# Kernel tuning notes

Hardware: AMD Instinct MI355X
Metric: run time of the kernel (lower is better)

Reference implementation:

```python
import jax, jax.numpy as jnp
import numpy as np

H = 32          # num_attention_heads
ROPE_BASE = 10000.0


def _rotary_freqs_cis(seq_len: int, head_dim: int) -> jnp.ndarray:
    # complex e^{i * pos * theta_j}, shape [seq_len, head_dim//2]
    inv_freq = 1.0 / (ROPE_BASE ** (jnp.arange(0, head_dim, 2, dtype=jnp.float32) / head_dim))
    angles = jnp.arange(seq_len, dtype=jnp.float32)[:, None] * inv_freq[None, :]
    return jax.lax.complex(jnp.cos(angles), jnp.sin(angles))


def _apply_rotary(u: jnp.ndarray, freqs_cis: jnp.ndarray) -> jnp.ndarray:
    # u: [B, S, H, hd]; faithful to apply_rotary_emb (interleaved pairs -> complex mul)
    ur = u.astype(jnp.float32).reshape(*u.shape[:-1], -1, 2)
    uc = jax.lax.complex(ur[..., 0], ur[..., 1])
    # freqs_cis broadcast: [1, S, 1, hd//2]
    uc = uc * freqs_cis[None, :, None, :]
    return jnp.stack((jnp.real(uc), jnp.imag(uc)), axis=-1).reshape(u.shape)


def setup_inputs() -> dict:
    key = jax.random.key(0)
    ks = jax.random.split(key, 5)
    B, S, D = 1, 2048, 4096
    init_std = 0.02
    x = jax.random.normal(ks[0], (B, S, D), dtype=jnp.float32)
    wq = jax.random.normal(ks[1], (D, D), dtype=jnp.float32) * init_std
    wk = jax.random.normal(ks[2], (D, D), dtype=jnp.float32) * init_std
    wv = jax.random.normal(ks[3], (D, D), dtype=jnp.float32) * init_std
    wo = jax.random.normal(ks[4], (D, D), dtype=jnp.float32) * init_std
    return {"x": x, "wq": wq, "wk": wk, "wv": wv, "wo": wo}


def reference(x, wq, wk, wv, wo):
    B, S, D = x.shape
    hd = D // H  # head_dim = 128
    q = (x @ wq).reshape(B, S, H, hd)
    k = (x @ wk).reshape(B, S, H, hd)
    v = (x @ wv).reshape(B, S, H, hd)

    freqs_cis = _rotary_freqs_cis(S, hd)
    q = _apply_rotary(q, freqs_cis)
    k = _apply_rotary(k, freqs_cis)
    # n_rep == 1 (num_key_value_heads == num_attention_heads) -> repeat_kv is identity

    scale = 1.0 / jnp.sqrt(jnp.float32(hd))
    scores = jnp.einsum('bqhd,bkhd->bhqk', q, k) * scale  # [B, H, S, S]
    causal = jnp.tril(jnp.ones((S, S), dtype=bool))
    neg = jnp.finfo(scores.dtype).min
    scores = jnp.where(causal[None, None, :, :], scores, neg)
    probs = jax.nn.softmax(scores, axis=-1)
    attn = jnp.einsum('bhqk,bkhd->bqhd', probs, v).reshape(B, S, D)
    return attn @ wo
```

## Files before the change

kernel.cpp:

```cpp
#include <hip/hip_runtime.h>
#include <stdint.h>

#define S_LEN 2048
#define DMODEL 4096
#define NHEAD 32
#define HDIM 128

typedef __attribute__((ext_vector_type(8))) short bf16x8;
typedef __attribute__((ext_vector_type(4))) float f32x4;

__device__ __forceinline__ unsigned short f2bf(float f) {
    union { float f; unsigned u; } v; v.f = f;
    unsigned u = v.u;
    unsigned r = (u + 0x7FFFu + ((u >> 16) & 1u)) >> 16;
    return (unsigned short)r;
}
__device__ __forceinline__ float bf2f(unsigned short h) {
    union { unsigned u; float f; } v; v.u = ((unsigned)h) << 16;
    return v.f;
}

__global__ void convert_x_kernel(const float* __restrict__ x,
                                 unsigned short* __restrict__ xb, int n4) {
    int t = blockIdx.x * blockDim.x + threadIdx.x;
    if (t >= n4) return;
    float4 v = ((const float4*)x)[t];
    ushort4 o;
    o.x = f2bf(v.x); o.y = f2bf(v.y); o.z = f2bf(v.z); o.w = f2bf(v.w);
    ((ushort4*)xb)[t] = o;
}

__global__ void convert_wt_kernel(const float* __restrict__ w,
                                  unsigned short* __restrict__ wt) {
    __shared__ unsigned short t[64][65];
    int n0 = blockIdx.x * 64, k0 = blockIdx.y * 64;
    for (int i = 0; i < 16; ++i) {
        int o = threadIdx.x + i * 256;
        int r = o >> 6, c = o & 63;
        t[r][c] = f2bf(w[(size_t)(k0 + r) * DMODEL + n0 + c]);
    }
    __syncthreads();
    for (int i = 0; i < 16; ++i) {
        int o = threadIdx.x + i * 256;
        int rr = o >> 6, kk = o & 63;
        wt[(size_t)(n0 + rr) * DMODEL + k0 + kk] = t[kk][rr];
    }
}

template<int STORE_MODE>
__global__ __launch_bounds__(256, 2)
void gemm_bt_kernel(const unsigned short* __restrict__ A,
                    const unsigned short* __restrict__ BT,
                    void* __restrict__ C, int M, int N, int K) {
    __shared__ __align__(16) unsigned short As[128 * 32];
    __shared__ __align__(16) unsigned short Bs[128 * 32];
    const int lane = threadIdx.x & 63;
    const int w = threadIdx.x >> 6;
    const int wm = w & 1, wn = w >> 1;
    const int m0 = blockIdx.y * 128, n0 = blockIdx.x * 128;

    f32x4 zero = {0.f, 0.f, 0.f, 0.f};
    f32x4 acc[4][4];
    for (int i = 0; i < 4; ++i)
        for (int j = 0; j < 4; ++j) acc[i][j] = zero;

    const int lr = lane >> 2;
    const int lc = lane & 3;
    const int q = lane >> 4, lm = lane & 15;

    for (int k0 = 0; k0 < K; k0 += 32) {
        __syncthreads();
        for (int i = 0; i < 2; ++i) {
            int rb = w * 32 + i * 16;
            int r = rb + lr;
            int gc = lc ^ ((r >> 1) & 3);
            const unsigned short* ga = A + (size_t)(m0 + r) * K + k0 + gc * 8;
            __builtin_amdgcn_global_load_lds(
                (__attribute__((address_space(1))) unsigned int*)ga,
                (__attribute__((address_space(3))) unsigned int*)(&As[rb * 32]), 16, 0, 0);
            const unsigned short* gb = BT + (size_t)(n0 + r) * K + k0 + gc * 8;
            __builtin_amdgcn_global_load_lds(
                (__attribute__((address_space(1))) unsigned int*)gb,
                (__attribute__((address_space(3))) unsigned int*)(&Bs[rb * 32]), 16, 0, 0);
        }
        __syncthreads();
        bf16x8 af[4], bf[4];
        for (int t = 0; t < 4; ++t) {
            int ra = wm * 64 + t * 16 + lm;
            af[t] = *(const bf16x8*)&As[ra * 32 + ((q ^ ((ra >> 1) & 3)) * 8)];
            int rb2 = wn * 64 + t * 16 + lm;
            bf[t] = *(const bf16x8*)&Bs[rb2 * 32 + ((q ^ ((rb2 >> 1) & 3)) * 8)];
        }
        for (int mi = 0; mi < 4; ++mi)
            for (int ni = 0; ni < 4; ++ni)
                acc[mi][ni] = __builtin_amdgcn_mfma_f32_16x16x32_bf16(
                    af[mi], bf[ni], acc[mi][ni], 0, 0, 0);
    }

    for (int mi = 0; mi < 4; ++mi) {
        int mbase = m0 + wm * 64 + mi * 16 + q * 4;
        for (int ni = 0; ni < 4; ++ni) {
            int n = n0 + wn * 64 + ni * 16 + lm;
            if (STORE_MODE == 0) {
                unsigned short* Cb = (unsigned short*)C;
                for (int r = 0; r < 4; ++r)
                    Cb[(size_t)(mbase + r) * N + n] = f2bf(acc[mi][ni][r]);
            } else if (STORE_MODE == 1) {
                unsigned short* Cb = (unsigned short*)C;
                ushort4 v;
                v.x = f2bf(acc[mi][ni][0]); v.y = f2bf(acc[mi][ni][1]);
                v.z = f2bf(acc[mi][ni][2]); v.w = f2bf(acc[mi][ni][3]);
                *(ushort4*)&Cb[(size_t)n * M + mbase] = v;
            } else {
                float* Cf = (float*)C;
                for (int r = 0; r < 4; ++r)
                    Cf[(size_t)(mbase + r) * N + n] = acc[mi][ni][r];
            }
        }
    }
}

__global__ void rope_kernel(unsigned short* __restrict__ qb,
                            unsigned short* __restrict__ kb) {
    int t = blockIdx.x * blockDim.x + threadIdx.x;
    if (t >= S_LEN * DMODEL / 2) return;
    int s = t >> 11;
    int p = t & 2047;
    int j = p & 63;
    float ang = (float)s * exp2f((float)j * -0.2076205059304602f);
    float sn, cs;
    sincosf(ang, &sn, &cs);
    size_t idx = (size_t)s * DMODEL + 2 * p;
    const float SC = 0.08838834764831845f;
    float a0 = bf2f(qb[idx]), a1 = bf2f(qb[idx + 1]);
    qb[idx]     = f2bf((a0 * cs - a1 * sn) * SC);
    qb[idx + 1] = f2bf((a0 * sn + a1 * cs) * SC);
    float b0 = bf2f(kb[idx]), b1 = bf2f(kb[idx + 1]);
    kb[idx]     = f2bf(b0 * cs - b1 * sn);
    kb[idx + 1] = f2bf(b0 * sn + b1 * cs);
}

__global__ __launch_bounds__(256, 2)
void attn_kernel(const unsigned short* __restrict__ qb,
                 const unsigned short* __restrict__ kb,
                 const unsigned short* __restrict__ vt,
                 unsigned short* __restrict__ ab) {
    __shared__ __align__(16) unsigned short Ks[64 * 128];
    __shared__ __align__(16) unsigned short VTs[128 * 64];
    __shared__ __align__(16) unsigned short Pb[4][16 * 72];
    const int t = threadIdx.x;
    const int lane = t & 63;
    const int w = t >> 6;
    const int h = blockIdx.y;
    const int q0 = ((int)gridDim.x - 1 - (int)blockIdx.x) * 64;
    const int qw = q0 + w * 16;
    const int q = lane >> 4, lm = lane & 15;

    const int krow = t >> 2;
    const int kcol = t & 3;
    const int vrow = t >> 1;
    const int vcol = t & 1;

    const unsigned short* gK = kb + (size_t)krow * DMODEL + h * HDIM;
    const unsigned short* gV = vt + (size_t)(h * HDIM + vrow) * S_LEN;

    bf16x8 qf[4];
    for (int kc = 0; kc < 4; ++kc)
        qf[kc] = *(const bf16x8*)&qb[(size_t)(qw + lm) * DMODEL + h * HDIM + kc * 32 + q * 8];

    f32x4 zero = {0.f, 0.f, 0.f, 0.f};
    f32x4 o[8];
    for (int i = 0; i < 8; ++i) o[i] = zero;
    float mrow[4] = {-1e30f, -1e30f, -1e30f, -1e30f};
    float lrow[4] = {0.f, 0.f, 0.f, 0.f};

    const int nch = q0 / 64 + 1;

    bf16x8 kreg[4], vreg[4];
    for (int i = 0; i < 4; ++i) {
        kreg[i] = *(const bf16x8*)&gK[(size_t)0 * DMODEL + (kcol + i * 4) * 8];
        vreg[i] = *(const bf16x8*)&gV[0 + (vcol + i * 2) * 8];
    }
    for (int i = 0; i < 4; ++i) {
        *(bf16x8*)&Ks[krow * 128 + (((kcol + i * 4) ^ (krow & 15)) * 8)] = kreg[i];
        *(bf16x8*)&VTs[vrow * 64 + (((vcol + i * 2) ^ (vrow & 7)) * 8)] = vreg[i];
    }
    __syncthreads();

    for (int c = 0; c < nch; ++c) {
        const int j0 = c * 64;
        if (c + 1 < nch) {
            const size_t jn = (size_t)(j0 + 64);
            for (int i = 0; i < 4; ++i) {
                kreg[i] = *(const bf16x8*)&gK[jn * DMODEL + (kcol + i * 4) * 8];
                vreg[i] = *(const bf16x8*)&gV[jn + (vcol + i * 2) * 8];
            }
        }

        f32x4 s[4];
        for (int ks = 0; ks < 4; ++ks) s[ks] = zero;
        for (int kc = 0; kc < 4; ++kc)
            for (int ks = 0; ks < 4; ++ks) {
                bf16x8 kf = *(const bf16x8*)&Ks[(ks * 16 + lm) * 128 + (((kc * 4 + q) ^ lm) * 8)];
                s[ks] = __builtin_amdgcn_mfma_f32_16x16x32_bf16(qf[kc], kf, s[ks], 0, 0, 0);
            }
        if (c == nch - 1) {
            for (int ks = 0; ks < 4; ++ks)
                for (int r = 0; r < 4; ++r)
                    if (j0 + ks * 16 + lm > qw + q * 4 + r) s[ks][r] = -1e30f;
        }
        float al[4];
        for (int r = 0; r < 4; ++r) {
            float mx = fmaxf(fmaxf(s[0][r], s[1][r]), fmaxf(s[2][r], s[3][r]));
            mx = fmaxf(mx, __shfl_xor(mx, 1));
            mx = fmaxf(mx, __shfl_xor(mx, 2));
            mx = fmaxf(mx, __shfl_xor(mx, 4));
            mx = fmaxf(mx, __shfl_xor(mx, 8));
            float mn = fmaxf(mrow[r], mx);
            al[r] = __expf(mrow[r] - mn);
            mrow[r] = mn;
            float rs = 0.f;
            float pv[4];
            for (int ks = 0; ks < 4; ++ks) {
                pv[ks] = __expf(s[ks][r] - mn);
                rs += pv[ks];
            }
            rs += __shfl_xor(rs, 1);
            rs += __shfl_xor(rs, 2);
            rs += __shfl_xor(rs, 4);
            rs += __shfl_xor(rs, 8);
            lrow[r] = lrow[r] * al[r] + rs;
            for (int ks = 0; ks < 4; ++ks)
                Pb[w][(q * 4 + r) * 72 + ks * 16 + lm] = f2bf(pv[ks]);
        }
        bf16x8 pA0 = *(const bf16x8*)&Pb[w][lm * 72 + q * 8];
        bf16x8 pA1 = *(const bf16x8*)&Pb[w][lm * 72 + 32 + q * 8];
        for (int nt = 0; nt < 8; ++nt) {
            int d = nt * 16 + lm;
            bf16x8 vf0 = *(const bf16x8*)&VTs[d * 64 + ((q ^ (d & 7)) * 8)];
            bf16x8 vf1 = *(const bf16x8*)&VTs[d * 64 + (((4 + q) ^ (d & 7)) * 8)];
            f32x4 oo = o[nt];
            for (int r = 0; r < 4; ++r) oo[r] *= al[r];
            oo = __builtin_amdgcn_mfma_f32_16x16x32_bf16(pA0, vf0, oo, 0, 0, 0);
            o[nt] = __builtin_amdgcn_mfma_f32_16x16x32_bf16(pA1, vf1, oo, 0, 0, 0);
        }

        __syncthreads();
        if (c + 1 < nch) {
            for (int i = 0; i < 4; ++i) {
                *(bf16x8*)&Ks[krow * 128 + (((kcol + i * 4) ^ (krow & 15)) * 8)] = kreg[i];
                *(bf16x8*)&VTs[vrow * 64 + (((vcol + i * 2) ^ (vrow & 7)) * 8)] = vreg[i];
            }
        }
        __syncthreads();
    }

    float inv[4];
    for (int r = 0; r < 4; ++r) inv[r] = 1.0f / lrow[r];
    for (int nt = 0; nt < 8; ++nt) {
        int d = h * HDIM + lm + nt * 16;
        for (int r = 0; r < 4; ++r)
            ab[(size_t)(qw + q * 4 + r) * DMODEL + d] = f2bf(o[nt][r] * inv[r]);
    }
}

extern "C" void kernel_launch(void* const* d_in, const int* in_sizes, int n_in,
                              void* d_out, int out_size, void* d_ws, size_t ws_size,
                              hipStream_t stream) {
    const float* x  = (const float*)d_in[0];
    const float* wq = (const float*)d_in[1];
    const float* wk = (const float*)d_in[2];
    const float* wv = (const float*)d_in[3];
    const float* wo = (const float*)d_in[4];
    char* ws = (char*)d_ws;
    const size_t MB = 1024 * 1024;
    unsigned short* xb  = (unsigned short*)(ws + 0 * MB);
    unsigned short* qb  = (unsigned short*)(ws + 16 * MB);
    unsigned short* kb  = (unsigned short*)(ws + 32 * MB);
    unsigned short* vtb = (unsigned short*)(ws + 48 * MB);
    unsigned short* ab  = (unsigned short*)(ws + 64 * MB);
    unsigned short* wtb = (unsigned short*)(ws + 80 * MB);

    dim3 cg(64, 64);
    dim3 gg(32, 16);

    convert_x_kernel<<<(S_LEN * DMODEL / 4) / 256, 256, 0, stream>>>(x, xb, S_LEN * DMODEL / 4);

    convert_wt_kernel<<<cg, 256, 0, stream>>>(wq, wtb);
    gemm_bt_kernel<0><<<gg, 256, 0, stream>>>(xb, wtb, qb, S_LEN, DMODEL, DMODEL);
    convert_wt_kernel<<<cg, 256, 0, stream>>>(wk, wtb);
    gemm_bt_kernel<0><<<gg, 256, 0, stream>>>(xb, wtb, kb, S_LEN, DMODEL, DMODEL);
    convert_wt_kernel<<<cg, 256, 0, stream>>>(wv, wtb);
    gemm_bt_kernel<1><<<gg, 256, 0, stream>>>(xb, wtb, vtb, S_LEN, DMODEL, DMODEL);

    rope_kernel<<<(S_LEN * DMODEL / 2) / 256, 256, 0, stream>>>(qb, kb);

    attn_kernel<<<dim3(S_LEN / 64, NHEAD), 256, 0, stream>>>(qb, kb, vtb, ab);

    convert_wt_kernel<<<cg, 256, 0, stream>>>(wo, wtb);
    gemm_bt_kernel<2><<<gg, 256, 0, stream>>>(ab, wtb, d_out, S_LEN, DMODEL, DMODEL);
}
```

Before: 803.6 us.

## Replace GEMM with 8-wave 256x128 double-buffered ping-pong pipelined kernel

Replaces the simple single-buffered 128x128 bf16 GEMM with a 512-thread kernel that computes 256x128 tiles with K=64 steps. Global-to-LDS loads for the next tiles are issued in stages and overlapped with MFMA phases, using explicit vmcnt waits, barriers, sched_barriers and setprio. Blocks are remapped so that consecutive blocks share B columns. The intent is to hide global load latency and raise MFMA utilisation in all four projection GEMMs. The cost is 96KB of dynamic LDS per block, which limits occupancy, and hand-tuned wait counts that must match the load schedule exactly.

```diff
diff --git a/kernel.cpp b/kernel.cpp
--- a/kernel.cpp
+++ b/kernel.cpp
@@ -47,60 +47,181 @@
     }
 }
 
+
+#define MFMA16(a, b, c) __builtin_amdgcn_mfma_f32_16x16x32_bf16(a, b, c, 0, 0, 0)
+
+#define GLDS(g, l) __builtin_amdgcn_global_load_lds( \
+    (__attribute__((address_space(1))) unsigned int*)(g), \
+    (__attribute__((address_space(3))) unsigned int*)(l), 16, 0, 0)
+
+#define VMCNT_(n) asm volatile("s_waitcnt vmcnt(" #n ")" ::: "memory")
+#define VMCNT(n) VMCNT_(n)
+
+#define PH_SYNC() \
+    __builtin_amdgcn_sched_barrier(0); \
+    __builtin_amdgcn_s_barrier(); \
+    asm volatile("s_waitcnt lgkmcnt(0)" ::: "memory"); \
+    __builtin_amdgcn_sched_barrier(0)
+
+#define PH_END() \
+    __builtin_amdgcn_s_setprio(0); \
+    __builtin_amdgcn_sched_barrier(0); \
+    __builtin_amdgcn_s_barrier(); \
+    __builtin_amdgcn_sched_barrier(0)
+
+#define PH_END_VM(VM) \
+    __builtin_amdgcn_s_setprio(0); \
+    __builtin_amdgcn_sched_barrier(0); \
+    VMCNT(VM); \
+    __builtin_amdgcn_s_barrier(); \
+    __builtin_amdgcn_sched_barrier(0)
+
+#define STAGE_A(T, PAR, J) do { \
+    size_t ko_ = (size_t)(T) * 64 + (J) * 32; \
+    GLDS(gA0 + ko_, As + ((PAR) * 2 + (J)) * 8192 + w * 512); \
+    GLDS(gA1 + ko_, As + ((PAR) * 2 + (J)) * 8192 + 4096 + w * 512); \
+} while (0)
+#define STAGE_B(T, PAR, J) do { \
+    size_t ko_ = (size_t)(T) * 64 + (J) * 32; \
+    GLDS(gB + ko_, Bs + ((PAR) * 2 + (J)) * 4096 + w * 512); \
+} while (0)
+
+#define TILE(T, P, S1, S2, VM2, VM4) do { \
+    const unsigned short* AsT = As + (P) * 16384; \
+    const unsigned short* BsT = Bs + (P) * 8192; \
+    bf16x8 af0, af1, af2, af3, bf0, bf1, bf2, bf3; \
+     \
+    af0 = *(const bf16x8*)&AsT[offA0]; \
+    af1 = *(const bf16x8*)&AsT[offA1]; \
+    af2 = *(const bf16x8*)&AsT[offA2]; \
+    af3 = *(const bf16x8*)&AsT[offA3]; \
+    bf0 = *(const bf16x8*)&BsT[offB0]; \
+    bf1 = *(const bf16x8*)&BsT[offB1]; \
+    if (S1) STAGE_A((T) + 1, (P) ^ 1, 1); \
+    PH_SYNC(); \
+    __builtin_amdgcn_s_setprio(1); \
+    acc[0][0] = MFMA16(af0, bf0, acc[0][0]); \
+    acc[1][0] = MFMA16(af1, bf0, acc[1][0]); \
+    acc[2][0] = MFMA16(af2, bf0, acc[2][0]); \
+    acc[3][0] = MFMA16(af3, bf0, acc[3][0]); \
+    acc[0][1] = MFMA16(af0, bf1, acc[0][1]); \
+    acc[1][1] = MFMA16(af1, bf1, acc[1][1]); \
+    acc[2][1] = MFMA16(af2, bf1, acc[2][1]); \
+    acc[3][1] = MFMA16(af3, bf1, acc[3][1]); \
+    PH_END(); \
+     \
+    bf2 = *(const bf16x8*)&BsT[offB2]; \
+    bf3 = *(const bf16x8*)&BsT[offB3]; \
+    if (S1) STAGE_B((T) + 1, (P) ^ 1, 1); \
+    PH_SYNC(); \
+    __builtin_amdgcn_s_setprio(1); \
+    acc[0][2] = MFMA16(af0, bf2, acc[0][2]); \
+    acc[1][2] = MFMA16(af1, bf2, acc[1][2]); \
+    acc[2][2] = MFMA16(af2, bf2, acc[2][2]); \
+    acc[3][2] = MFMA16(af3, bf2, acc[3][2]); \
+    acc[0][3] = MFMA16(af0, bf3, acc[0][3]); \
+    acc[1][3] = MFMA16(af1, bf3, acc[1][3]); \
+    acc[2][3] = MFMA16(af2, bf3, acc[2][3]); \
+    acc[3][3] = MFMA16(af3, bf3, acc[3][3]); \
+    PH_END_VM(VM2); \
+     \
+    af0 = *(const bf16x8*)&AsT[8192 + offA0]; \
+    af1 = *(const bf16x8*)&AsT[8192 + offA1]; \
+    af2 = *(const bf16x8*)&AsT[8192 + offA2]; \
+    af3 = *(const bf16x8*)&AsT[8192 + offA3]; \
+    bf0 = *(const bf16x8*)&BsT[4096 + offB0]; \
+    bf1 = *(const bf16x8*)&BsT[4096 + offB1]; \
+    if (S2) STAGE_A((T) + 2, (P), 0); \
+    PH_SYNC(); \
+    __builtin_amdgcn_s_setprio(1); \
+    acc[0][0] = MFMA16(af0, bf0, acc[0][0]); \
+    acc[1][0] = MFMA16(af1, bf0, acc[1][0]); \
+    acc[2][0] = MFMA16(af2, bf0, acc[2][0]); \
+    acc[3][0] = MFMA16(af3, bf0, acc[3][0]); \
+    acc[0][1] = MFMA16(af0, bf1, acc[0][1]); \
+    acc[1][1] = MFMA16(af1, bf1, acc[1][1]); \
+    acc[2][1] = MFMA16(af2, bf1, acc[2][1]); \
+    acc[3][1] = MFMA16(af3, bf1, acc[3][1]); \
+    PH_END(); \
+     \
+    bf2 = *(const bf16x8*)&BsT[4096 + offB2]; \
+    bf3 = *(const bf16x8*)&BsT[4096 + offB3]; \
+    if (S2) STAGE_B((T) + 2, (P), 0); \
+    PH_SYNC(); \
+    __builtin_amdgcn_s_setprio(1); \
+    acc[0][2] = MFMA16(af0, bf2, acc[0][2]); \
+    acc[1][2] = MFMA16(af1, bf2, acc[1][2]); \
+    acc[2][2] = MFMA16(af2, bf2, acc[2][2]); \
+    acc[3][2] = MFMA16(af3, bf2, acc[3][2]); \
+    acc[0][3] = MFMA16(af0, bf3, acc[0][3]); \
+    acc[1][3] = MFMA16(af1, bf3, acc[1][3]); \
+    acc[2][3] = MFMA16(af2, bf3, acc[2][3]); \
+    acc[3][3] = MFMA16(af3, bf3, acc[3][3]); \
+    PH_END_VM(VM4); \
+} while (0)
+
 template<int STORE_MODE>
-__global__ __launch_bounds__(256, 2)
-void gemm_bt_kernel(const unsigned short* __restrict__ A,
-                    const unsigned short* __restrict__ BT,
-                    void* __restrict__ C, int M, int N, int K) {
-    __shared__ __align__(16) unsigned short As[128 * 32];
-    __shared__ __align__(16) unsigned short Bs[128 * 32];
-    const int lane = threadIdx.x & 63;
-    const int w = threadIdx.x >> 6;
-    const int wm = w & 1, wn = w >> 1;
-    const int m0 = blockIdx.y * 128, n0 = blockIdx.x * 128;
+__global__ __launch_bounds__(512, 2)
+void gemm8p_kernel(const unsigned short* __restrict__ A,
+                   const unsigned short* __restrict__ BT,
+                   void* __restrict__ C) {
+    constexpr int M = S_LEN, N = DMODEL, K = DMODEL;
+    constexpr int NT = K / 64;
+    extern __shared__ __align__(16) unsigned short sm[];
+    unsigned short* As = sm;
+    unsigned short* Bs = sm + 32768;
+
+    const int tid = threadIdx.x;
+    const int lane = tid & 63;
+    const int w = tid >> 6;
+    const int wr = w >> 1, wc = w & 1;
+    const int q = lane >> 4, lm = lane & 15;
+
+    int orig = blockIdx.y * gridDim.x + blockIdx.x;
+    const int by = orig & 7;
+    const int bx = orig >> 3;
+    const int m0 = by * 256, n0 = bx * 128;
+
+    const int c4 = tid & 3, r4 = tid >> 2, s4 = (tid >> 3) & 3;
+    const unsigned short* gA0 = A + (size_t)(m0 + r4) * K + ((c4 ^ s4) * 8);
+    const unsigned short* gA1 = gA0 + (size_t)128 * K;
+    const unsigned short* gB  = BT + (size_t)(n0 + r4) * K + ((c4 ^ s4) * 8);
+
+#define FRAGOFF(r_) ((r_) * 32 + ((q ^ (((r_) >> 1) & 3)) * 8))
+    const int rA = wr * 64 + lm, rB = wc * 64 + lm;
+    const int offA0 = FRAGOFF(rA);
+    const int offA1 = FRAGOFF(rA + 16);
+    const int offA2 = FRAGOFF(rA + 32);
+    const int offA3 = FRAGOFF(rA + 48);
+    const int offB0 = FRAGOFF(rB);
+    const int offB1 = FRAGOFF(rB + 16);
+    const int offB2 = FRAGOFF(rB + 32);
+    const int offB3 = FRAGOFF(rB + 48);
+#undef FRAGOFF
 
     f32x4 zero = {0.f, 0.f, 0.f, 0.f};
     f32x4 acc[4][4];
     for (int i = 0; i < 4; ++i)
         for (int j = 0; j < 4; ++j) acc[i][j] = zero;
 
-    const int lr = lane >> 2;
-    const int lc = lane & 3;
-    const int q = lane >> 4, lm = lane & 15;
-
-    for (int k0 = 0; k0 < K; k0 += 32) {
-        __syncthreads();
-        for (int i = 0; i < 2; ++i) {
-            int rb = w * 32 + i * 16;
-            int r = rb + lr;
-            int gc = lc ^ ((r >> 1) & 3);
-            const unsigned short* ga = A + (size_t)(m0 + r) * K + k0 + gc * 8;
-            __builtin_amdgcn_global_load_lds(
-                (__attribute__((address_space(1))) unsigned int*)ga,
-                (__attribute__((address_space(3))) unsigned int*)(&As[rb * 32]), 16, 0, 0);
-            const unsigned short* gb = BT + (size_t)(n0 + r) * K + k0 + gc * 8;
-            __builtin_amdgcn_global_load_lds(
-                (__attribute__((address_space(1))) unsigned int*)gb,
-                (__attribute__((address_space(3))) unsigned int*)(&Bs[rb * 32]), 16, 0, 0);
-        }
-        __syncthreads();
-        bf16x8 af[4], bf[4];
-        for (int t = 0; t < 4; ++t) {
-            int ra = wm * 64 + t * 16 + lm;
-            af[t] = *(const bf16x8*)&As[ra * 32 + ((q ^ ((ra >> 1) & 3)) * 8)];
-            int rb2 = wn * 64 + t * 16 + lm;
-            bf[t] = *(const bf16x8*)&Bs[rb2 * 32 + ((q ^ ((rb2 >> 1) & 3)) * 8)];
-        }
-        for (int mi = 0; mi < 4; ++mi)
-            for (int ni = 0; ni < 4; ++ni)
-                acc[mi][ni] = __builtin_amdgcn_mfma_f32_16x16x32_bf16(
-                    af[mi], bf[ni], acc[mi][ni], 0, 0, 0);
-    }
+    STAGE_A(0, 0, 0); STAGE_B(0, 0, 0);
+    STAGE_A(0, 0, 1); STAGE_B(0, 0, 1);
+    STAGE_A(1, 1, 0); STAGE_B(1, 1, 0);
+    VMCNT(6);
+    __builtin_amdgcn_s_barrier();
+    __builtin_amdgcn_sched_barrier(0);
+
+    for (int t = 0; t < NT - 2; t += 2) {
+        TILE(t, 0, true, true, 6, 6);
+        TILE(t + 1, 1, true, true, 6, 6);
+    }
+    TILE(NT - 2, 0, true, false, 6, 3);
+    TILE(NT - 1, 1, false, false, 0, 0);
 
     for (int mi = 0; mi < 4; ++mi) {
-        int mbase = m0 + wm * 64 + mi * 16 + q * 4;
+        int mbase = m0 + wr * 64 + mi * 16 + q * 4;
         for (int ni = 0; ni < 4; ++ni) {
-            int n = n0 + wn * 64 + ni * 16 + lm;
+            int n = n0 + wc * 64 + ni * 16 + lm;
             if (STORE_MODE == 0) {
                 unsigned short* Cb = (unsigned short*)C;
                 for (int r = 0; r < 4; ++r)
@@ -281,22 +402,33 @@
     unsigned short* ab  = (unsigned short*)(ws + 64 * MB);
     unsigned short* wtb = (unsigned short*)(ws + 80 * MB);
 
+    static int attr_done = 0;
+    if (!attr_done) {
+        hipFuncSetAttribute((const void*)&gemm8p_kernel<0>,
+                            hipFuncAttributeMaxDynamicSharedMemorySize, 98304);
+        hipFuncSetAttribute((const void*)&gemm8p_kernel<1>,
+                            hipFuncAttributeMaxDynamicSharedMemorySize, 98304);
+        hipFuncSetAttribute((const void*)&gemm8p_kernel<2>,
+                            hipFuncAttributeMaxDynamicSharedMemorySize, 98304);
+        attr_done = 1;
+    }
+
     dim3 cg(64, 64);
-    dim3 gg(32, 16);
+    dim3 gg(32, 8);
 
     convert_x_kernel<<<(S_LEN * DMODEL / 4) / 256, 256, 0, stream>>>(x, xb, S_LEN * DMODEL / 4);
 
     convert_wt_kernel<<<cg, 256, 0, stream>>>(wq, wtb);
-    gemm_bt_kernel<0><<<gg, 256, 0, stream>>>(xb, wtb, qb, S_LEN, DMODEL, DMODEL);
+    gemm8p_kernel<0><<<gg, 512, 98304, stream>>>(xb, wtb, qb);
     convert_wt_kernel<<<cg, 256, 0, stream>>>(wk, wtb);
-    gemm_bt_kernel<0><<<gg, 256, 0, stream>>>(xb, wtb, kb, S_LEN, DMODEL, DMODEL);
+    gemm8p_kernel<0><<<gg, 512, 98304, stream>>>(xb, wtb, kb);
     convert_wt_kernel<<<cg, 256, 0, stream>>>(wv, wtb);
-    gemm_bt_kernel<1><<<gg, 256, 0, stream>>>(xb, wtb, vtb, S_LEN, DMODEL, DMODEL);
+    gemm8p_kernel<1><<<gg, 512, 98304, stream>>>(xb, wtb, vtb);
 
     rope_kernel<<<(S_LEN * DMODEL / 2) / 256, 256, 0, stream>>>(qb, kb);
 
     attn_kernel<<<dim3(S_LEN / 64, NHEAD), 256, 0, stream>>>(qb, kb, vtb, ab);
 
     convert_wt_kernel<<<cg, 256, 0, stream>>>(wo, wtb);
-    gemm_bt_kernel<2><<<gg, 256, 0, stream>>>(ab, wtb, d_out, S_LEN, DMODEL, DMODEL);
-}
+    gemm8p_kernel<2><<<gg, 512, 98304, stream>>>(ab, wtb, d_out);
+}
```

Result: faster. 728.0 us (-9.4%).
